# Kernel optimization log

Measured on AMD Instinct MI355X. Metric: run time of the kernel, lower is better.

Reference implementation:

```python
import jax, jax.numpy as jnp
import numpy as np

T = 2.0          # hardcoded in the original __init__ (ignores the arg)
EPSILON = 0.1
N_ITERS = 20     # sinkhorn_loss passes n_iters=20 to sinkhorn_normalized
SCALE = 0.001


def setup_inputs() -> dict:
    key = jax.random.key(0)
    k1, k2 = jax.random.split(key)
    B, N, C = 8, 1024, 64
    y_s = jax.random.normal(k1, (B, N, C), dtype=jnp.float32)
    y_t = jax.random.normal(k2, (B, N, C), dtype=jnp.float32)
    return {"y_s": y_s, "y_t": y_t}


def _sinkhorn_loss(x, y):
    # x, y: [N, C]. cdist p=1 -> [N, N]
    Wxy = jnp.sum(jnp.abs(x[:, None, :] - y[None, :, :]), axis=-1)  # [N, N]
    K = jnp.exp(-Wxy / EPSILON)

    def body(P, _):
        P = P / jnp.sum(P, axis=1, keepdims=True)  # row normalize
        P = P / jnp.sum(P, axis=0, keepdims=True)  # col normalize
        return P, None

    P, _ = jax.lax.scan(body, K, None, length=N_ITERS)
    return jnp.sum(P * Wxy)


def reference(y_s, y_t):
    # softmax over dim=1 (the N axis), exactly as nn.Softmax(dim=1) on [B,N,C]
    p_s = jax.nn.softmax(y_s / T, axis=1)
    p_t = jax.nn.softmax(y_t / T, axis=1)
    # original Python loop computes the loss per sample but OVERWRITES
    # emd_loss each iteration; lax.map mirrors the sequential per-sample
    # work, and we return only the last sample's loss (faithful to the bug).
    losses = jax.lax.map(lambda xy: _sinkhorn_loss(xy[0], xy[1]), (p_s, p_t))
    return SCALE * losses[-1]
```

## Files before the change

### kernel.cpp

```cpp
#include <hip/hip_runtime.h>


static constexpr int N = 1024;
static constexpr int C = 64;

static constexpr int WS_XS  = 0;
static constexpr int WS_YS  = 65536;
static constexpr int WS_K   = 131072;
static constexpr int WS_KT  = 1179648;
static constexpr int WS_ULL = 2228224;
static constexpr int WS_VLL = 2230272;
static constexpr int WS_PLL = 2232320;

typedef float    f32x4 __attribute__((ext_vector_type(4)));
typedef unsigned u32x4 __attribute__((ext_vector_type(4)));
typedef unsigned u32x2 __attribute__((ext_vector_type(2)));

__device__ __forceinline__ float wsum(float v) {
    #pragma unroll
    for (int o = 32; o > 0; o >>= 1) v += __shfl_down(v, o, 64);
    return v;
}
__device__ __forceinline__ float wmax(float v) {
    #pragma unroll
    for (int o = 32; o > 0; o >>= 1) v = fmaxf(v, __shfl_down(v, o, 64));
    return v;
}

__device__ __forceinline__ void ll_write(float* unit, float val, unsigned g) {
    u32x2 d;
    d.x = __float_as_uint(val);
    d.y = g;
    asm volatile("global_store_dwordx2 %0, %1, off sc0 sc1"
                 :: "v"(unit), "v"(d) : "memory");
}

__device__ __forceinline__ void ll_read4(const float* buf, unsigned g,
                                         float* sv, int t) {
    const float* p = buf + t * 8;
    u32x4 a, b;
    for (;;) {
        asm volatile(
            "global_load_dwordx4 %0, %2, off sc0 sc1\n\t"
            "global_load_dwordx4 %1, %2, off offset:16 sc0 sc1\n\t"
            "s_waitcnt vmcnt(0)"
            : "=&v"(a), "=&v"(b) : "v"(p) : "memory");
        if (a.y == g && a.w == g && b.y == g && b.w == g) break;
        __builtin_amdgcn_s_sleep(1);
    }
    const int u0 = t * 4;
    sv[u0 + 0] = __uint_as_float(a.x);
    sv[u0 + 1] = __uint_as_float(a.z);
    sv[u0 + 2] = __uint_as_float(b.x);
    sv[u0 + 3] = __uint_as_float(b.z);
}

__global__ void __launch_bounds__(256)
softmax_k(const float* __restrict__ ysrc, const float* __restrict__ ytrc,
          float* __restrict__ ws)
{
    __shared__ float sm[4];
    const int tid = threadIdx.x, bid = blockIdx.x;
    const int wid = tid >> 6, lane = tid & 63;
    const float* src = ((bid < C) ? ysrc : ytrc) + 7 * N * C;
    float* dst = ws + ((bid < C) ? WS_XS : WS_YS);
    const int c = bid & (C - 1);

    float vals[4];
    float m = -1e30f;
    #pragma unroll
    for (int q = 0; q < 4; ++q) {
        vals[q] = src[(q * 256 + tid) * C + c] * 0.5f;
        m = fmaxf(m, vals[q]);
    }
    m = wmax(m);
    if (lane == 0) sm[wid] = m;
    __syncthreads();
    m = fmaxf(fmaxf(sm[0], sm[1]), fmaxf(sm[2], sm[3]));
    float s = 0.f;
    #pragma unroll
    for (int q = 0; q < 4; ++q) { vals[q] = expf(vals[q] - m); s += vals[q]; }
    s = wsum(s);
    __syncthreads();
    if (lane == 0) sm[wid] = s;
    __syncthreads();
    s = sm[0] + sm[1] + sm[2] + sm[3];
    const float inv = 1.0f / s;
    #pragma unroll
    for (int q = 0; q < 4; ++q) dst[(q * 256 + tid) * C + c] = vals[q] * inv;
}

__global__ void __launch_bounds__(256)
buildK_k(float* __restrict__ ws)
{
    __shared__ float smem[5184];
    float* xs  = ws + WS_XS;
    float* ysm = ws + WS_YS;
    float* K   = ws + WS_K;
    float* KT  = ws + WS_KT;
    const int tid = threadIdx.x, bid = blockIdx.x;

    if (bid < 4) ws[WS_VLL + (bid * 256 + tid) * 2] = 1.0f;

    float* sx = smem;
    float* sy = smem + 2048;
    float* kt = smem + 4128;
    #pragma unroll 1
    for (int t = 0; t < 4; ++t) {
        const int tt = bid * 4 + t;
        const int ti = tt >> 5, tj = tt & 31;
        __syncthreads();
        for (int k = tid; k < 2048; k += 256) sx[k] = xs[ti * 2048 + k];
        for (int k = tid; k < 2048; k += 256)
            sy[(k >> 6) * 65 + (k & 63)] = ysm[tj * 2048 + k];
        __syncthreads();
        float kv[4];
        #pragma unroll
        for (int q = 0; q < 4; ++q) {
            const int idx = q * 256 + tid;
            const int il = idx >> 5, jl = idx & 31;
            float a = 0.f;
            #pragma unroll
            for (int c2 = 0; c2 < 64; ++c2)
                a += fabsf(sx[il * 64 + c2] - sy[jl * 65 + c2]);
            kv[q] = expf(-10.0f * a);
            K[(ti * 32 + il) * N + tj * 32 + jl] = kv[q];
        }
        __syncthreads();
        #pragma unroll
        for (int q = 0; q < 4; ++q) {
            const int idx = q * 256 + tid;
            kt[(idx >> 5) * 33 + (idx & 31)] = kv[q];
        }
        __syncthreads();
        #pragma unroll
        for (int q = 0; q < 4; ++q) {
            const int idx = q * 256 + tid;
            const int jl = idx >> 5, il = idx & 31;
            KT[(tj * 32 + jl) * N + ti * 32 + il] = kt[il * 33 + jl];
        }
    }
}

__global__ void __launch_bounds__(256)
sinkhorn_loop_k(float* __restrict__ ws, float* __restrict__ out)
{
    __shared__ __align__(16) float rows[32 * 1024];
    __shared__ __align__(16) float sv[1024];
    __shared__ float stage[16];
    __shared__ float fsm[4];
    const int tid = threadIdx.x, bid = blockIdx.x;
    const int wid = tid >> 6, lane = tid & 63;

    {
        const f32x4* Ksrc  = (const f32x4*)(ws + WS_K  + bid * 16 * N);
        const f32x4* KTsrc = (const f32x4*)(ws + WS_KT + bid * 16 * N);
        f32x4* dK  = (f32x4*)rows;
        f32x4* dKT = (f32x4*)(rows + 16 * N);
        #pragma unroll 4
        for (int q = 0; q < 16; ++q) dK[tid + 256 * q]  = Ksrc[tid + 256 * q];
        #pragma unroll 4
        for (int q = 0; q < 16; ++q) dKT[tid + 256 * q] = KTsrc[tid + 256 * q];
    }
    __syncthreads();

    float* uLL = ws + WS_ULL;
    float* vLL = ws + WS_VLL;
    float* pLL = ws + WS_PLL;
    const float* rK  = rows + (wid * 4) * N;
    const float* rKT = rows + 16 * N + (wid * 4) * N;
    float u_s[4];
    unsigned g = 0;

    #pragma unroll 1
    for (int it = 0; it < 20; ++it) {
        ll_read4(vLL, g, sv, tid);
        __syncthreads();
        #pragma unroll
        for (int s = 0; s < 4; ++s) {
            const f32x4* Kr = (const f32x4*)(rK + s * N);
            const f32x4 k0 = Kr[lane], k1 = Kr[lane + 64],
                        k2 = Kr[lane + 128], k3 = Kr[lane + 192];
            const f32x4 b0 = *(const f32x4*)&sv[(lane) * 4];
            const f32x4 b1 = *(const f32x4*)&sv[(lane + 64) * 4];
            const f32x4 b2 = *(const f32x4*)&sv[(lane + 128) * 4];
            const f32x4 b3 = *(const f32x4*)&sv[(lane + 192) * 4];
            float acc = 0.f;
            acc += k0.x * b0.x + k0.y * b0.y + k0.z * b0.z + k0.w * b0.w;
            acc += k1.x * b1.x + k1.y * b1.y + k1.z * b1.z + k1.w * b1.w;
            acc += k2.x * b2.x + k2.y * b2.y + k2.z * b2.z + k2.w * b2.w;
            acc += k3.x * b3.x + k3.y * b3.y + k3.z * b3.z + k3.w * b3.w;
            acc = wsum(acc);
            if (lane == 0) { u_s[s] = 1.0f / acc; stage[wid * 4 + s] = u_s[s]; }
        }
        __syncthreads();
        ++g;
        if (tid < 16) ll_write(uLL + (bid * 16 + tid) * 2, stage[tid], g);

        ll_read4(uLL, g, sv, tid);
        __syncthreads();
        #pragma unroll
        for (int s = 0; s < 4; ++s) {
            const f32x4* Kr = (const f32x4*)(rKT + s * N);
            const f32x4 k0 = Kr[lane], k1 = Kr[lane + 64],
                        k2 = Kr[lane + 128], k3 = Kr[lane + 192];
            const f32x4 b0 = *(const f32x4*)&sv[(lane) * 4];
            const f32x4 b1 = *(const f32x4*)&sv[(lane + 64) * 4];
            const f32x4 b2 = *(const f32x4*)&sv[(lane + 128) * 4];
            const f32x4 b3 = *(const f32x4*)&sv[(lane + 192) * 4];
            float acc = 0.f;
            acc += k0.x * b0.x + k0.y * b0.y + k0.z * b0.z + k0.w * b0.w;
            acc += k1.x * b1.x + k1.y * b1.y + k1.z * b1.z + k1.w * b1.w;
            acc += k2.x * b2.x + k2.y * b2.y + k2.z * b2.z + k2.w * b2.w;
            acc += k3.x * b3.x + k3.y * b3.y + k3.z * b3.z + k3.w * b3.w;
            acc = wsum(acc);
            if (lane == 0) stage[wid * 4 + s] = 1.0f / acc;
        }
        __syncthreads();
        ++g;
        if (tid < 16) ll_write(vLL + (bid * 16 + tid) * 2, stage[tid], g);
    }

    ll_read4(vLL, g, sv, tid);
    __syncthreads();
    {
        float p = 0.f;
        #pragma unroll
        for (int s = 0; s < 4; ++s) {
            const float* Kr = rK + s * N;
            float acc = 0.f;
            for (int j = lane; j < N; j += 64) {
                const float kk = Kr[j];
                acc += kk * sv[j] * logf(kk);
            }
            acc = wsum(acc);
            if (lane == 0) p += u_s[s] * acc;
        }
        if (lane == 0) ll_write(pLL + (bid * 4 + wid) * 2, p, 41u);
    }

    if (bid == 0) {
        const float* pp = pLL + tid * 2;
        u32x2 c;
        for (;;) {
            asm volatile("global_load_dwordx2 %0, %1, off sc0 sc1\n\t"
                         "s_waitcnt vmcnt(0)"
                         : "=&v"(c) : "v"(pp) : "memory");
            if (c.y == 41u) break;
            __builtin_amdgcn_s_sleep(1);
        }
        float acc = __uint_as_float(c.x);
        acc = wsum(acc);
        if (lane == 0) fsm[wid] = acc;
        __syncthreads();
        if (tid == 0)
            out[0] = -1e-4f * (fsm[0] + fsm[1] + fsm[2] + fsm[3]);
    }
}

extern "C" void kernel_launch(void* const* d_in, const int* in_sizes, int n_in,
                              void* d_out, int out_size, void* d_ws, size_t ws_size,
                              hipStream_t stream) {
    const float* y_s = (const float*)d_in[0];
    const float* y_t = (const float*)d_in[1];
    float* ws = (float*)d_ws;

    hipMemsetAsync((char*)d_ws + (size_t)WS_ULL * sizeof(float), 0,
                   (size_t)(2048 + 2048 + 512) * sizeof(float), stream);
    softmax_k<<<dim3(128), dim3(256), 0, stream>>>(y_s, y_t, ws);
    buildK_k<<<dim3(256), dim3(256), 0, stream>>>(ws);
    sinkhorn_loop_k<<<dim3(64), dim3(256), 0, stream>>>(ws, (float*)d_out);
}
```

Measured before the change: 200.2 us.

## Double-buffer scaling vectors to drop barriers; vectorize buildK distance loads

The Sinkhorn loop now writes each wave's results straight to the global flag buffers from lane 0. It no longer stages them in shared memory behind a barrier. Alternating shared buffers (svA/svB) for the u and v vectors remove two __syncthreads per iteration. buildK_k switches to vectorized float4 loads into padded shared tiles and keeps each thread's y row in registers, cutting LDS traffic in the L1 distance computation. The ll_read4 store also becomes a single float4 write. The risk is correctness with double buffering, and higher register pressure from the 16 float4 y registers.

```diff
diff --git a/kernel.cpp b/kernel.cpp
--- a/kernel.cpp
+++ b/kernel.cpp
@@ -48,11 +48,12 @@
         if (a.y == g && a.w == g && b.y == g && b.w == g) break;
         __builtin_amdgcn_s_sleep(1);
     }
-    const int u0 = t * 4;
-    sv[u0 + 0] = __uint_as_float(a.x);
-    sv[u0 + 1] = __uint_as_float(a.z);
-    sv[u0 + 2] = __uint_as_float(b.x);
-    sv[u0 + 3] = __uint_as_float(b.z);
+    f32x4 vv;
+    vv.x = __uint_as_float(a.x);
+    vv.y = __uint_as_float(a.z);
+    vv.z = __uint_as_float(b.x);
+    vv.w = __uint_as_float(b.z);
+    *(f32x4*)&sv[t * 4] = vv;
 }
 
 __global__ void __launch_bounds__(256)
@@ -93,36 +94,54 @@
 __global__ void __launch_bounds__(256)
 buildK_k(float* __restrict__ ws)
 {
-    __shared__ float smem[5184];
+    __shared__ __align__(16) float sx[32 * 64];
+    __shared__ __align__(16) float sy[32 * 68];
+    __shared__ float kt[32 * 33];
     float* xs  = ws + WS_XS;
     float* ysm = ws + WS_YS;
     float* K   = ws + WS_K;
     float* KT  = ws + WS_KT;
     const int tid = threadIdx.x, bid = blockIdx.x;
+    const int jl = tid & 31;
 
     if (bid < 4) ws[WS_VLL + (bid * 256 + tid) * 2] = 1.0f;
 
-    float* sx = smem;
-    float* sy = smem + 2048;
-    float* kt = smem + 4128;
     #pragma unroll 1
     for (int t = 0; t < 4; ++t) {
         const int tt = bid * 4 + t;
         const int ti = tt >> 5, tj = tt & 31;
         __syncthreads();
-        for (int k = tid; k < 2048; k += 256) sx[k] = xs[ti * 2048 + k];
-        for (int k = tid; k < 2048; k += 256)
-            sy[(k >> 6) * 65 + (k & 63)] = ysm[tj * 2048 + k];
-        __syncthreads();
+        {
+            const f32x4* xsrc = (const f32x4*)(xs + ti * 2048);
+            f32x4* dx = (f32x4*)sx;
+            dx[tid]       = xsrc[tid];
+            dx[tid + 256] = xsrc[tid + 256];
+            const f32x4* ysrc = (const f32x4*)(ysm + tj * 2048);
+            #pragma unroll
+            for (int h = 0; h < 2; ++h) {
+                const int k4 = tid + h * 256;
+                const int row = k4 >> 4, c4 = k4 & 15;
+                *(f32x4*)&sy[row * 68 + c4 * 4] = ysrc[k4];
+            }
+        }
+        __syncthreads();
+        f32x4 yr[16];
+        #pragma unroll
+        for (int c4 = 0; c4 < 16; ++c4)
+            yr[c4] = *(const f32x4*)&sy[jl * 68 + c4 * 4];
         float kv[4];
         #pragma unroll
         for (int q = 0; q < 4; ++q) {
-            const int idx = q * 256 + tid;
-            const int il = idx >> 5, jl = idx & 31;
+            const int il = (q * 256 + tid) >> 5;
             float a = 0.f;
             #pragma unroll
-            for (int c2 = 0; c2 < 64; ++c2)
-                a += fabsf(sx[il * 64 + c2] - sy[jl * 65 + c2]);
+            for (int c4 = 0; c4 < 16; ++c4) {
+                const f32x4 xv = *(const f32x4*)&sx[il * 64 + c4 * 4];
+                a += fabsf(xv.x - yr[c4].x);
+                a += fabsf(xv.y - yr[c4].y);
+                a += fabsf(xv.z - yr[c4].z);
+                a += fabsf(xv.w - yr[c4].w);
+            }
             kv[q] = expf(-10.0f * a);
             K[(ti * 32 + il) * N + tj * 32 + jl] = kv[q];
         }
@@ -136,8 +155,8 @@
         #pragma unroll
         for (int q = 0; q < 4; ++q) {
             const int idx = q * 256 + tid;
-            const int jl = idx >> 5, il = idx & 31;
-            KT[(tj * 32 + jl) * N + ti * 32 + il] = kt[il * 33 + jl];
+            const int jl2 = idx >> 5, il2 = idx & 31;
+            KT[(tj * 32 + jl2) * N + ti * 32 + il2] = kt[il2 * 33 + jl2];
         }
     }
 }
@@ -146,8 +165,8 @@
 sinkhorn_loop_k(float* __restrict__ ws, float* __restrict__ out)
 {
     __shared__ __align__(16) float rows[32 * 1024];
-    __shared__ __align__(16) float sv[1024];
-    __shared__ float stage[16];
+    __shared__ __align__(16) float svA[1024];
+    __shared__ __align__(16) float svB[1024];
     __shared__ float fsm[4];
     const int tid = threadIdx.x, bid = blockIdx.x;
     const int wid = tid >> 6, lane = tid & 63;
@@ -169,59 +188,60 @@
     float* pLL = ws + WS_PLL;
     const float* rK  = rows + (wid * 4) * N;
     const float* rKT = rows + 16 * N + (wid * 4) * N;
+    const int ub = (bid * 16 + wid * 4) * 2;
     float u_s[4];
     unsigned g = 0;
 
     #pragma unroll 1
     for (int it = 0; it < 20; ++it) {
-        ll_read4(vLL, g, sv, tid);
-        __syncthreads();
+        ll_read4(vLL, g, svA, tid);
+        __syncthreads();
+        ++g;
         #pragma unroll
         for (int s = 0; s < 4; ++s) {
             const f32x4* Kr = (const f32x4*)(rK + s * N);
             const f32x4 k0 = Kr[lane], k1 = Kr[lane + 64],
                         k2 = Kr[lane + 128], k3 = Kr[lane + 192];
-            const f32x4 b0 = *(const f32x4*)&sv[(lane) * 4];
-            const f32x4 b1 = *(const f32x4*)&sv[(lane + 64) * 4];
-            const f32x4 b2 = *(const f32x4*)&sv[(lane + 128) * 4];
-            const f32x4 b3 = *(const f32x4*)&sv[(lane + 192) * 4];
+            const f32x4 b0 = *(const f32x4*)&svA[(lane) * 4];
+            const f32x4 b1 = *(const f32x4*)&svA[(lane + 64) * 4];
+            const f32x4 b2 = *(const f32x4*)&svA[(lane + 128) * 4];
+            const f32x4 b3 = *(const f32x4*)&svA[(lane + 192) * 4];
             float acc = 0.f;
             acc += k0.x * b0.x + k0.y * b0.y + k0.z * b0.z + k0.w * b0.w;
             acc += k1.x * b1.x + k1.y * b1.y + k1.z * b1.z + k1.w * b1.w;
             acc += k2.x * b2.x + k2.y * b2.y + k2.z * b2.z + k2.w * b2.w;
             acc += k3.x * b3.x + k3.y * b3.y + k3.z * b3.z + k3.w * b3.w;
             acc = wsum(acc);
-            if (lane == 0) { u_s[s] = 1.0f / acc; stage[wid * 4 + s] = u_s[s]; }
-        }
+            if (lane == 0) {
+                u_s[s] = 1.0f / acc;
+                ll_write(uLL + ub + s * 2, u_s[s], g);
+            }
+        }
+
+        ll_read4(uLL, g, svB, tid);
         __syncthreads();
         ++g;
-        if (tid < 16) ll_write(uLL + (bid * 16 + tid) * 2, stage[tid], g);
-
-        ll_read4(uLL, g, sv, tid);
-        __syncthreads();
         #pragma unroll
         for (int s = 0; s < 4; ++s) {
             const f32x4* Kr = (const f32x4*)(rKT + s * N);
             const f32x4 k0 = Kr[lane], k1 = Kr[lane + 64],
                         k2 = Kr[lane + 128], k3 = Kr[lane + 192];
-            const f32x4 b0 = *(const f32x4*)&sv[(lane) * 4];
-            const f32x4 b1 = *(const f32x4*)&sv[(lane + 64) * 4];
-            const f32x4 b2 = *(const f32x4*)&sv[(lane + 128) * 4];
-            const f32x4 b3 = *(const f32x4*)&sv[(lane + 192) * 4];
+            const f32x4 b0 = *(const f32x4*)&svB[(lane) * 4];
+            const f32x4 b1 = *(const f32x4*)&svB[(lane + 64) * 4];
+            const f32x4 b2 = *(const f32x4*)&svB[(lane + 128) * 4];
+            const f32x4 b3 = *(const f32x4*)&svB[(lane + 192) * 4];
             float acc = 0.f;
             acc += k0.x * b0.x + k0.y * b0.y + k0.z * b0.z + k0.w * b0.w;
             acc += k1.x * b1.x + k1.y * b1.y + k1.z * b1.z + k1.w * b1.w;
             acc += k2.x * b2.x + k2.y * b2.y + k2.z * b2.z + k2.w * b2.w;
             acc += k3.x * b3.x + k3.y * b3.y + k3.z * b3.z + k3.w * b3.w;
             acc = wsum(acc);
-            if (lane == 0) stage[wid * 4 + s] = 1.0f / acc;
-        }
-        __syncthreads();
-        ++g;
-        if (tid < 16) ll_write(vLL + (bid * 16 + tid) * 2, stage[tid], g);
-    }
-
-    ll_read4(vLL, g, sv, tid);
+            if (lane == 0)
+                ll_write(vLL + ub + s * 2, 1.0f / acc, g);
+        }
+    }
+
+    ll_read4(vLL, g, svA, tid);
     __syncthreads();
     {
         float p = 0.f;
@@ -231,7 +251,7 @@
             float acc = 0.f;
             for (int j = lane; j < N; j += 64) {
                 const float kk = Kr[j];
-                acc += kk * sv[j] * logf(kk);
+                acc += kk * svA[j] * logf(kk);
             }
             acc = wsum(acc);
             if (lane == 0) p += u_s[s] * acc;
```

Result: slower. 220.8 us (+10.3%).
